# Kernel optimization log

Hardware: AMD Instinct MI355X
Metric: run time of the kernel (lower is better)

## Reference

```python
import jax, jax.numpy as jnp
import numpy as np

BN_EPS = 1e-5

def _tok2img(f):
    # f: [197, 768] tokens (CLS first). Drop CLS, transpose, reshape -> [1, 768, 14, 14].
    # fv4[0, c, i, j] = f[1 + i*14 + j, c], identical to the original triple loop.
    return f[1:].T.reshape(1, 768, 14, 14)

def _resize(x, s):
    # PyTorch F.interpolate(mode='bilinear', align_corners=False) == jax.image.resize 'bilinear'
    n, c, h, w = x.shape
    return jax.image.resize(x, (n, c, h * s, w * s), method='bilinear')

def _conv_relu_bn(x, conv_w, conv_b, g, b, m, v):
    y = jax.lax.conv_general_dilated(x, conv_w, window_strides=(1, 1), padding='SAME',
                                     dimension_numbers=('NCHW', 'OIHW', 'NCHW'))
    y = y + conv_b[None, :, None, None]
    y = jax.nn.relu(y)
    # BatchNorm2d(1) in eval mode with running stats
    scale = g * jax.lax.rsqrt(v + BN_EPS)
    return y * scale[None, :, None, None] + (b - m * scale)[None, :, None, None]

def setup_inputs() -> dict:
    key = jax.random.key(0)
    ks = jax.random.split(key, 4)
    return {
        'x': jax.random.normal(ks[0], (14, 14), dtype=jnp.float32),
        'fv': jax.random.normal(ks[1], (4, 197, 768), dtype=jnp.float32),
        'conv_w': jax.random.normal(ks[2], (1, 769, 3, 3), dtype=jnp.float32) * 0.02,
        'conv_b': jnp.zeros((1,), jnp.float32),
        'bn_gamma': jnp.ones((1,), jnp.float32),
        'bn_beta': jnp.zeros((1,), jnp.float32),
        'bn_mean': jnp.zeros((1,), jnp.float32),
        'bn_var': jnp.ones((1,), jnp.float32),
        'W_w': jax.random.normal(ks[3], (224, 224), dtype=jnp.float32) * 0.05,
        'W_b': jnp.zeros((224,), jnp.float32),
    }

def reference(x, fv, conv_w, conv_b, bn_gamma, bn_beta, bn_mean, bn_var, W_w, W_b):
    h = x[None, None]  # [1,1,14,14]
    # skip features, pre-resized to match current resolution at each stage
    feats = (
        _tok2img(fv[3]),              # 14x14
        _resize(_tok2img(fv[2]), 2),  # 28x28
        _resize(_tok2img(fv[1]), 4),  # 56x56
        _resize(_tok2img(fv[0]), 8),  # 112x112
    )
    for f in feats:
        h = jnp.concatenate([h, f], axis=1)  # [1,769,H,W]
        h = _conv_relu_bn(h, conv_w, conv_b, bn_gamma, bn_beta, bn_mean, bn_var)
        h = _resize(h, 2)
    # Linear(224,224) over the last dim of [1,1,224,224]
    h = jnp.einsum('nchw,ow->ncho', h, W_w) + W_b
    return jax.nn.sigmoid(h)
```

## Files before the change

kernel.cpp:

```cpp
#include <hip/hip_runtime.h>
#include <math.h>


#define BN_EPS 1e-5f

__device__ __forceinline__ float clampf(float x, float lo, float hi) {
    return fminf(fmaxf(x, lo), hi);
}

__device__ __forceinline__ float sampleB(const float* __restrict__ Bt, float fy, float fx) {
    int y0 = (int)fy; float by = fy - (float)y0; int y1 = min(y0 + 1, 13);
    int x0 = (int)fx; float bx = fx - (float)x0; int x1 = min(x0 + 1, 13);
    return (1.f - by) * ((1.f - bx) * Bt[y0 * 14 + x0] + bx * Bt[y0 * 14 + x1])
         + by         * ((1.f - bx) * Bt[y1 * 14 + x0] + bx * Bt[y1 * 14 + x1]);
}

__device__ __forceinline__ float stage_pixel(int i, int j, int H,
                                             const float* __restrict__ hsrc, int srcH,
                                             const float* __restrict__ sB,
                                             const float* __restrict__ cw, float bias) {
    float featScale = 14.0f / (float)H;
    float srcMax = (float)(srcH - 1);
    float acc = bias;

#pragma unroll
    for (int a = 0; a < 3; ++a) {
        int p = i + a - 1;
        if (p < 0 || p >= H) continue;
        float fy = clampf(((float)p + 0.5f) * featScale - 0.5f, 0.f, 13.f);
        float hy = clampf(((float)p + 0.5f) * 0.5f - 0.5f, 0.f, srcMax);
        int hy0 = (int)hy; float fhy = hy - (float)hy0; int hy1 = min(hy0 + 1, srcH - 1);
#pragma unroll
        for (int bq = 0; bq < 3; ++bq) {
            int q = j + bq - 1;
            if (q < 0 || q >= H) continue;
            int t = a * 3 + bq;

            float fx = clampf(((float)q + 0.5f) * featScale - 0.5f, 0.f, 13.f);
            float bv = sampleB(sB + t * 196, fy, fx);

            float hx = clampf(((float)q + 0.5f) * 0.5f - 0.5f, 0.f, srcMax);
            int hx0 = (int)hx; float fhx = hx - (float)hx0; int hx1 = min(hx0 + 1, srcH - 1);
            float hval = (1.f - fhy) * ((1.f - fhx) * hsrc[hy0 * srcH + hx0] + fhx * hsrc[hy0 * srcH + hx1])
                       + fhy         * ((1.f - fhx) * hsrc[hy1 * srcH + hx0] + fhx * hsrc[hy1 * srcH + hx1]);
            acc += cw[t] * hval + bv;
        }
    }
    return acc;
}

__device__ __forceinline__ void srcRange(int dlo, int dhi, int srcH, int& slo, int& shi) {
    int H = 2 * srcH;
    int p0 = max(dlo - 1, 0), p1 = min(dhi + 1, H - 1);
    float h0 = fmaxf(((float)p0 + 0.5f) * 0.5f - 0.5f, 0.f);
    float h1 = fmaxf(((float)p1 + 0.5f) * 0.5f - 0.5f, 0.f);
    slo = (int)h0;
    shi = min((int)h1 + 1, srcH - 1);
}

__device__ __forceinline__ void bRange(int dlo, int dhi, int H, int& lo, int& hi) {
    float sc = 14.f / (float)H;
    int p0 = max(dlo - 1, 0), p1 = min(dhi + 1, H - 1);
    float f0 = clampf(((float)p0 + 0.5f) * sc - 0.5f, 0.f, 13.f);
    float f1 = clampf(((float)p1 + 0.5f) * sc - 0.5f, 0.f, 13.f);
    lo = (int)f0;
    hi = min((int)f1 + 1, 13);
}

__global__ __launch_bounds__(256)
void compute_B_kernel(const float* __restrict__ fv, const float* __restrict__ conv_w,
                      const float* __restrict__ W_w,
                      float* __restrict__ gB, float* __restrict__ gWTf) {
    int blk = blockIdx.x;
    int s = blk / 196;
    int uv = blk % 196;
    const float* fvrow = fv + ((size_t)(3 - s) * 197 + 1 + uv) * 768;
    int tid = threadIdx.x;

    if (tid < 32) {
        int idx = blk * 32 + tid;
        int o = idx % 224, xx = idx / 224;
        float acc = 0.f;
#pragma unroll
        for (int d = -1; d <= 2; ++d) {
            int w = 2 * xx + d;
            if (w < 0 || w > 223) continue;
            float hx = clampf(((float)w + 0.5f) * 0.5f - 0.5f, 0.f, 111.f);
            int xx0 = (int)hx; float fx = hx - (float)xx0; int xx1 = min(xx0 + 1, 111);
            float c = (xx0 == xx ? 1.f - fx : 0.f) + (xx1 == xx ? fx : 0.f);
            acc += c * W_w[o * 224 + w];
        }
        gWTf[xx * 224 + o] = acc;
    }

    float part[9];
#pragma unroll
    for (int t = 0; t < 9; ++t) part[t] = 0.f;
    for (int k = tid; k < 768; k += 256) {
        float fval = fvrow[k];
        const float* w = conv_w + (size_t)(1 + k) * 9;
#pragma unroll
        for (int t = 0; t < 9; ++t) part[t] += fval * w[t];
    }
#pragma unroll
    for (int t = 0; t < 9; ++t) {
#pragma unroll
        for (int off = 32; off > 0; off >>= 1)
            part[t] += __shfl_down(part[t], off, 64);
    }
    __shared__ float red[4][9];
    int wave = tid >> 6, lane = tid & 63;
    if (lane == 0) {
#pragma unroll
        for (int t = 0; t < 9; ++t) red[wave][t] = part[t];
    }
    __syncthreads();
    if (tid < 9)
        gB[s * 1764 + tid * 196 + uv] = red[0][tid] + red[1][tid] + red[2][tid] + red[3][tid];
}

__global__ __launch_bounds__(1024, 1)
void refine_kernel(const float* __restrict__ x,
                   const float* __restrict__ conv_w, const float* __restrict__ conv_b,
                   const float* __restrict__ bng, const float* __restrict__ bnb,
                   const float* __restrict__ bnm, const float* __restrict__ bnv,
                   const float* __restrict__ W_b,
                   const float* __restrict__ gB, const float* __restrict__ gWTf,
                   float* __restrict__ out) {
    __shared__ float sB[4 * 9 * 196];
    __shared__ float y1s[196];
    __shared__ float y2s[784];
    __shared__ float y3s[3136];
    __shared__ float y4loc[3 * 112];
    __shared__ float partial[12 * 224];

    int tid = threadIdx.x;
    int b = blockIdx.x;

    int y4lo = max(b - 1, 0), y4hi = min(b + 1, 111);
    int r3lo, r3hi; srcRange(y4lo, y4hi, 56, r3lo, r3hi);
    int r2lo, r2hi; srcRange(r3lo, r3hi, 28, r2lo, r2hi);
    int r1lo, r1hi; srcRange(r2lo, r2hi, 14, r1lo, r1hi);

    int bl0 = max(r1lo - 1, 0), bh0 = min(r1hi + 1, 13);
    int bl1, bh1; bRange(r2lo, r2hi, 28, bl1, bh1);
    int bl2, bh2; bRange(r3lo, r3hi, 56, bl2, bh2);
    int bl3, bh3; bRange(y4lo, y4hi, 112, bl3, bh3);

    {
        int bl[4] = {bl0, bl1, bl2, bl3}, bh[4] = {bh0, bh1, bh2, bh3};
#pragma unroll
        for (int s4 = 0; s4 < 4; ++s4) {
            int nrw = (bh[s4] - bl[s4] + 1) * 14;
            int n = 9 * nrw;
            int base = s4 * 1764 + bl[s4] * 14;
            for (int e = tid; e < n; e += 1024) {
                int t = e / nrw, rem = e % nrw;
                int off = base + t * 196 + rem;
                sB[off] = gB[off];
            }
        }
    }

    float cw[9];
#pragma unroll
    for (int t = 0; t < 9; ++t) cw[t] = conv_w[t];
    float bias = conv_b[0];
    float scale = bng[0] * rsqrtf(bnv[0] + BN_EPS);
    float shift = bnb[0] - bnm[0] * scale;
    __syncthreads();

    {
        int n = (r1hi - r1lo + 1) * 14;
        if (tid < n) {
            int i = r1lo + tid / 14, j = tid % 14;
            float acc = bias;
#pragma unroll
            for (int a = 0; a < 3; ++a) {
                int p = i + a - 1;
                if (p < 0 || p >= 14) continue;
#pragma unroll
                for (int bq = 0; bq < 3; ++bq) {
                    int q = j + bq - 1;
                    if (q < 0 || q >= 14) continue;
                    int t = a * 3 + bq;
                    acc += cw[t] * x[p * 14 + q] + sB[t * 196 + p * 14 + q];
                }
            }
            y1s[i * 14 + j] = fmaxf(acc, 0.f) * scale + shift;
        }
    }
    __syncthreads();

    {
        int n = (r2hi - r2lo + 1) * 28;
        if (tid < n) {
            int i = r2lo + tid / 28, j = tid % 28;
            float acc = stage_pixel(i, j, 28, y1s, 14, sB + 1764, cw, bias);
            y2s[i * 28 + j] = fmaxf(acc, 0.f) * scale + shift;
        }
    }
    __syncthreads();

    {
        int n = (r3hi - r3lo + 1) * 56;
        if (tid < n) {
            int i = r3lo + tid / 56, j = tid % 56;
            float acc = stage_pixel(i, j, 56, y2s, 28, sB + 2 * 1764, cw, bias);
            y3s[i * 56 + j] = fmaxf(acc, 0.f) * scale + shift;
        }
    }
    __syncthreads();

    {
        int n = (y4hi - y4lo + 1) * 112;
        if (tid < n) {
            int i = y4lo + tid / 112, j = tid % 112;
            float acc = stage_pixel(i, j, 112, y3s, 56, sB + 3 * 1764, cw, bias);
            y4loc[(i - (b - 1)) * 112 + j] = fmaxf(acc, 0.f) * scale + shift;
        }
    }
    __syncthreads();

    if (tid < 896) {
        int kq = tid / 224, o = tid % 224;
        int k0 = kq * 28;
        float a0 = 0.f, a1 = 0.f, a2 = 0.f;
        for (int k = k0; k < k0 + 28; ++k) {
            float wf = gWTf[k * 224 + o];
            a0 += y4loc[k] * wf;
            a1 += y4loc[112 + k] * wf;
            a2 += y4loc[224 + k] * wf;
        }
        partial[(0 * 4 + kq) * 224 + o] = a0;
        partial[(1 * 4 + kq) * 224 + o] = a1;
        partial[(2 * 4 + kq) * 224 + o] = a2;
    }
    __syncthreads();

    if (tid < 448) {
        int rr = tid / 224, o = tid % 224;
        int r = 2 * b + rr;
        float hy = clampf(((float)r + 0.5f) * 0.5f - 0.5f, 0.f, 111.f);
        int yy0 = (int)hy; float fy = hy - (float)yy0; int yy1 = min(yy0 + 1, 111);
        int s0 = yy0 - (b - 1), s1 = yy1 - (b - 1);
        float D0 = partial[(s0 * 4 + 0) * 224 + o] + partial[(s0 * 4 + 1) * 224 + o]
                 + partial[(s0 * 4 + 2) * 224 + o] + partial[(s0 * 4 + 3) * 224 + o];
        float D1 = partial[(s1 * 4 + 0) * 224 + o] + partial[(s1 * 4 + 1) * 224 + o]
                 + partial[(s1 * 4 + 2) * 224 + o] + partial[(s1 * 4 + 3) * 224 + o];
        float v = (1.f - fy) * D0 + fy * D1 + W_b[o];
        out[(size_t)r * 224 + o] = 1.f / (1.f + expf(-v));
    }
}

extern "C" void kernel_launch(void* const* d_in, const int* in_sizes, int n_in,
                              void* d_out, int out_size, void* d_ws, size_t ws_size,
                              hipStream_t stream) {
    (void)in_sizes; (void)n_in; (void)out_size; (void)ws_size;
    const float* x      = (const float*)d_in[0];
    const float* fv     = (const float*)d_in[1];
    const float* conv_w = (const float*)d_in[2];
    const float* conv_b = (const float*)d_in[3];
    const float* bng    = (const float*)d_in[4];
    const float* bnb    = (const float*)d_in[5];
    const float* bnm    = (const float*)d_in[6];
    const float* bnv    = (const float*)d_in[7];
    const float* W_w    = (const float*)d_in[8];
    const float* W_b    = (const float*)d_in[9];
    float* out = (float*)d_out;

    float* ws   = (float*)d_ws;
    float* gB   = ws;
    float* gWTf = ws + 7056;

    compute_B_kernel<<<784, 256, 0, stream>>>(fv, conv_w, W_w, gB, gWTf);
    refine_kernel<<<112, 1024, 0, stream>>>(x, conv_w, conv_b, bng, bnb, bnm, bnv,
                                            W_b, gB, gWTf, out);
}
```

Measured before the change: 86.86 us.

## Fuse feature-projection precompute into refine kernel via cooperative grid sync

The separate compute_B kernel is merged into the refine kernel. Each of the 112 blocks computes seven feature-token projections and its own row of the folded linear weights, writes them to workspace, then waits on a cooperative grid-wide barrier before the refinement stages run. This removes a second kernel launch and the gap between launches. In exchange it depends on cooperative launch, pays for a grid sync, and uses fewer, larger blocks for the projection work.

```diff
diff --git a/kernel.cpp b/kernel.cpp
--- a/kernel.cpp
+++ b/kernel.cpp
@@ -1,5 +1,8 @@
 #include <hip/hip_runtime.h>
+#include <hip/hip_cooperative_groups.h>
 #include <math.h>
+
+namespace cg = cooperative_groups;
 
 
 #define BN_EPS 1e-5f
@@ -67,75 +70,77 @@
     hi = min((int)f1 + 1, 13);
 }
 
-__global__ __launch_bounds__(256)
-void compute_B_kernel(const float* __restrict__ fv, const float* __restrict__ conv_w,
-                      const float* __restrict__ W_w,
-                      float* __restrict__ gB, float* __restrict__ gWTf) {
-    int blk = blockIdx.x;
-    int s = blk / 196;
-    int uv = blk % 196;
-    const float* fvrow = fv + ((size_t)(3 - s) * 197 + 1 + uv) * 768;
-    int tid = threadIdx.x;
-
-    if (tid < 32) {
-        int idx = blk * 32 + tid;
-        int o = idx % 224, xx = idx / 224;
-        float acc = 0.f;
-#pragma unroll
-        for (int d = -1; d <= 2; ++d) {
-            int w = 2 * xx + d;
-            if (w < 0 || w > 223) continue;
-            float hx = clampf(((float)w + 0.5f) * 0.5f - 0.5f, 0.f, 111.f);
-            int xx0 = (int)hx; float fx = hx - (float)xx0; int xx1 = min(xx0 + 1, 111);
-            float c = (xx0 == xx ? 1.f - fx : 0.f) + (xx1 == xx ? fx : 0.f);
-            acc += c * W_w[o * 224 + w];
-        }
-        gWTf[xx * 224 + o] = acc;
-    }
-
-    float part[9];
-#pragma unroll
-    for (int t = 0; t < 9; ++t) part[t] = 0.f;
-    for (int k = tid; k < 768; k += 256) {
-        float fval = fvrow[k];
-        const float* w = conv_w + (size_t)(1 + k) * 9;
-#pragma unroll
-        for (int t = 0; t < 9; ++t) part[t] += fval * w[t];
-    }
-#pragma unroll
-    for (int t = 0; t < 9; ++t) {
-#pragma unroll
-        for (int off = 32; off > 0; off >>= 1)
-            part[t] += __shfl_down(part[t], off, 64);
-    }
-    __shared__ float red[4][9];
-    int wave = tid >> 6, lane = tid & 63;
-    if (lane == 0) {
-#pragma unroll
-        for (int t = 0; t < 9; ++t) red[wave][t] = part[t];
-    }
-    __syncthreads();
-    if (tid < 9)
-        gB[s * 1764 + tid * 196 + uv] = red[0][tid] + red[1][tid] + red[2][tid] + red[3][tid];
-}
-
 __global__ __launch_bounds__(1024, 1)
-void refine_kernel(const float* __restrict__ x,
-                   const float* __restrict__ conv_w, const float* __restrict__ conv_b,
-                   const float* __restrict__ bng, const float* __restrict__ bnb,
-                   const float* __restrict__ bnm, const float* __restrict__ bnv,
-                   const float* __restrict__ W_b,
-                   const float* __restrict__ gB, const float* __restrict__ gWTf,
-                   float* __restrict__ out) {
+void refine_fused(const float* __restrict__ x, const float* __restrict__ fv,
+                  const float* __restrict__ conv_w, const float* __restrict__ conv_b,
+                  const float* __restrict__ bng, const float* __restrict__ bnb,
+                  const float* __restrict__ bnm, const float* __restrict__ bnv,
+                  const float* __restrict__ W_w, const float* __restrict__ W_b,
+                  float* __restrict__ gB, float* __restrict__ gWTf,
+                  float* __restrict__ out) {
     __shared__ float sB[4 * 9 * 196];
     __shared__ float y1s[196];
     __shared__ float y2s[784];
     __shared__ float y3s[3136];
     __shared__ float y4loc[3 * 112];
     __shared__ float partial[12 * 224];
+    __shared__ float red[14][9];
 
     int tid = threadIdx.x;
     int b = blockIdx.x;
+
+    if (tid < 896) {
+        int e7 = tid >> 7, r = tid & 127;
+        int e = b * 7 + e7;
+        int s = e / 196, uv = e % 196;
+        const float* fvrow = fv + ((size_t)(3 - s) * 197 + 1 + uv) * 768;
+        float part[9];
+#pragma unroll
+        for (int t = 0; t < 9; ++t) part[t] = 0.f;
+#pragma unroll
+        for (int i = 0; i < 6; ++i) {
+            int c = r + 128 * i;
+            float fval = fvrow[c];
+            const float* w = conv_w + (size_t)(1 + c) * 9;
+#pragma unroll
+            for (int t = 0; t < 9; ++t) part[t] += fval * w[t];
+        }
+#pragma unroll
+        for (int t = 0; t < 9; ++t) {
+#pragma unroll
+            for (int off = 32; off > 0; off >>= 1)
+                part[t] += __shfl_down(part[t], off, 64);
+        }
+        if ((tid & 63) == 0) {
+            int wv = tid >> 6;
+#pragma unroll
+            for (int t = 0; t < 9; ++t) red[wv][t] = part[t];
+        }
+    }
+
+    if (tid < 224) {
+        int o = tid;
+        float acc = 0.f;
+#pragma unroll
+        for (int d = -1; d <= 2; ++d) {
+            int w = 2 * b + d;
+            if (w < 0 || w > 223) continue;
+            float hx = clampf(((float)w + 0.5f) * 0.5f - 0.5f, 0.f, 111.f);
+            int xx0 = (int)hx; float fx = hx - (float)xx0; int xx1 = min(xx0 + 1, 111);
+            float c = (xx0 == b ? 1.f - fx : 0.f) + (xx1 == b ? fx : 0.f);
+            acc += c * W_w[o * 224 + w];
+        }
+        gWTf[b * 224 + o] = acc;
+    }
+    __syncthreads();
+    if (tid < 63) {
+        int e7 = tid / 9, t = tid - e7 * 9;
+        int e = b * 7 + e7;
+        int s = e / 196, uv = e % 196;
+        gB[s * 1764 + t * 196 + uv] = red[2 * e7][t] + red[2 * e7 + 1][t];
+    }
+
+    cg::this_grid().sync();
 
     int y4lo = max(b - 1, 0), y4hi = min(b + 1, 111);
     int r3lo, r3hi; srcRange(y4lo, y4hi, 56, r3lo, r3hi);
@@ -273,7 +278,11 @@
     float* gB   = ws;
     float* gWTf = ws + 7056;
 
-    compute_B_kernel<<<784, 256, 0, stream>>>(fv, conv_w, W_w, gB, gWTf);
-    refine_kernel<<<112, 1024, 0, stream>>>(x, conv_w, conv_b, bng, bnb, bnm, bnv,
-                                            W_b, gB, gWTf, out);
-}
+    void* args[13] = {
+        (void*)&x, (void*)&fv, (void*)&conv_w, (void*)&conv_b,
+        (void*)&bng, (void*)&bnb, (void*)&bnm, (void*)&bnv,
+        (void*)&W_w, (void*)&W_b, (void*)&gB, (void*)&gWTf, (void*)&out
+    };
+    hipLaunchCooperativeKernel((void*)refine_fused, dim3(112), dim3(1024),
+                               args, 0, stream);
+}
```

Result: slower. 118.9 us (+36.9%).

## Fuse B and W-transform precompute into a single refine kernel

Applied to the files above, without the earlier changes.

Drops the separate precompute kernel. Each of the 112 blocks now computes only the feature-projection (B) entries its row window needs, one wave per token row with conv weights held in registers. It also builds the resized linear-weight matrix in shared memory instead of reading it from global workspace. This removes a kernel launch and the global round trip for intermediates. In exchange it adds redundant per-block recomputation, a large shared-memory footprint and heavy register pressure from the 108-element weight cache.

```diff
diff --git a/kernel.cpp b/kernel.cpp
--- a/kernel.cpp
+++ b/kernel.cpp
@@ -67,75 +67,24 @@
     hi = min((int)f1 + 1, 13);
 }
 
-__global__ __launch_bounds__(256)
-void compute_B_kernel(const float* __restrict__ fv, const float* __restrict__ conv_w,
-                      const float* __restrict__ W_w,
-                      float* __restrict__ gB, float* __restrict__ gWTf) {
-    int blk = blockIdx.x;
-    int s = blk / 196;
-    int uv = blk % 196;
-    const float* fvrow = fv + ((size_t)(3 - s) * 197 + 1 + uv) * 768;
-    int tid = threadIdx.x;
-
-    if (tid < 32) {
-        int idx = blk * 32 + tid;
-        int o = idx % 224, xx = idx / 224;
-        float acc = 0.f;
-#pragma unroll
-        for (int d = -1; d <= 2; ++d) {
-            int w = 2 * xx + d;
-            if (w < 0 || w > 223) continue;
-            float hx = clampf(((float)w + 0.5f) * 0.5f - 0.5f, 0.f, 111.f);
-            int xx0 = (int)hx; float fx = hx - (float)xx0; int xx1 = min(xx0 + 1, 111);
-            float c = (xx0 == xx ? 1.f - fx : 0.f) + (xx1 == xx ? fx : 0.f);
-            acc += c * W_w[o * 224 + w];
-        }
-        gWTf[xx * 224 + o] = acc;
-    }
-
-    float part[9];
-#pragma unroll
-    for (int t = 0; t < 9; ++t) part[t] = 0.f;
-    for (int k = tid; k < 768; k += 256) {
-        float fval = fvrow[k];
-        const float* w = conv_w + (size_t)(1 + k) * 9;
-#pragma unroll
-        for (int t = 0; t < 9; ++t) part[t] += fval * w[t];
-    }
-#pragma unroll
-    for (int t = 0; t < 9; ++t) {
-#pragma unroll
-        for (int off = 32; off > 0; off >>= 1)
-            part[t] += __shfl_down(part[t], off, 64);
-    }
-    __shared__ float red[4][9];
-    int wave = tid >> 6, lane = tid & 63;
-    if (lane == 0) {
-#pragma unroll
-        for (int t = 0; t < 9; ++t) red[wave][t] = part[t];
-    }
-    __syncthreads();
-    if (tid < 9)
-        gB[s * 1764 + tid * 196 + uv] = red[0][tid] + red[1][tid] + red[2][tid] + red[3][tid];
-}
-
 __global__ __launch_bounds__(1024, 1)
-void refine_kernel(const float* __restrict__ x,
-                   const float* __restrict__ conv_w, const float* __restrict__ conv_b,
-                   const float* __restrict__ bng, const float* __restrict__ bnb,
-                   const float* __restrict__ bnm, const float* __restrict__ bnv,
-                   const float* __restrict__ W_b,
-                   const float* __restrict__ gB, const float* __restrict__ gWTf,
-                   float* __restrict__ out) {
+void refine_one(const float* __restrict__ x, const float* __restrict__ fv,
+                const float* __restrict__ conv_w, const float* __restrict__ conv_b,
+                const float* __restrict__ bng, const float* __restrict__ bnb,
+                const float* __restrict__ bnm, const float* __restrict__ bnv,
+                const float* __restrict__ W_w, const float* __restrict__ W_b,
+                float* __restrict__ out) {
     __shared__ float sB[4 * 9 * 196];
     __shared__ float y1s[196];
     __shared__ float y2s[784];
     __shared__ float y3s[3136];
     __shared__ float y4loc[3 * 112];
     __shared__ float partial[12 * 224];
+    __shared__ float sWTf[112 * 224];
 
     int tid = threadIdx.x;
     int b = blockIdx.x;
+    int wave = tid >> 6, lane = tid & 63;
 
     int y4lo = max(b - 1, 0), y4hi = min(b + 1, 111);
     int r3lo, r3hi; srcRange(y4lo, y4hi, 56, r3lo, r3hi);
@@ -147,17 +96,49 @@
     int bl2, bh2; bRange(r3lo, r3hi, 56, bl2, bh2);
     int bl3, bh3; bRange(y4lo, y4hi, 112, bl3, bh3);
 
-    {
-        int bl[4] = {bl0, bl1, bl2, bl3}, bh[4] = {bh0, bh1, bh2, bh3};
-#pragma unroll
-        for (int s4 = 0; s4 < 4; ++s4) {
-            int nrw = (bh[s4] - bl[s4] + 1) * 14;
-            int n = 9 * nrw;
-            int base = s4 * 1764 + bl[s4] * 14;
-            for (int e = tid; e < n; e += 1024) {
-                int t = e / nrw, rem = e % nrw;
-                int off = base + t * 196 + rem;
-                sB[off] = gB[off];
+    int n0  = (bh0 - bl0 + 1) * 14;
+    int n1p = (bh1 - bl1 + 1) * 14;
+    int n2p = (bh2 - bl2 + 1) * 14;
+    int n3p = (bh3 - bl3 + 1) * 14;
+    int off1 = n0, off2 = n0 + n1p, off3 = n0 + n1p + n2p;
+    int Ne = off3 + n3p;
+
+    float cwreg[12][9];
+#pragma unroll
+    for (int i = 0; i < 12; ++i) {
+        const float* wp = conv_w + (size_t)(1 + lane + 64 * i) * 9;
+#pragma unroll
+        for (int t = 0; t < 9; ++t) cwreg[i][t] = wp[t];
+    }
+
+    {
+        int chunk = (Ne + 15) >> 4;
+        int e0 = wave * chunk, e1 = min(e0 + chunk, Ne);
+        for (int e = e0; e < e1; ++e) {
+            int s = (e >= off1) + (e >= off2) + (e >= off3);
+            int base = (s == 0) ? 0   : (s == 1) ? off1 : (s == 2) ? off2 : off3;
+            int bls  = (s == 0) ? bl0 : (s == 1) ? bl1  : (s == 2) ? bl2  : bl3;
+            int uv = bls * 14 + (e - base);
+            const float* fvrow = fv + ((size_t)(3 - s) * 197 + 1 + uv) * 768 + lane;
+            float acc[9];
+#pragma unroll
+            for (int t = 0; t < 9; ++t) acc[t] = 0.f;
+#pragma unroll
+            for (int i = 0; i < 12; ++i) {
+                float f = fvrow[64 * i];
+#pragma unroll
+                for (int t = 0; t < 9; ++t) acc[t] += cwreg[i][t] * f;
+            }
+#pragma unroll
+            for (int t = 0; t < 9; ++t) {
+#pragma unroll
+                for (int off = 32; off > 0; off >>= 1)
+                    acc[t] += __shfl_down(acc[t], off, 64);
+            }
+            if (lane == 0) {
+                int db = s * 1764 + uv;
+#pragma unroll
+                for (int t = 0; t < 9; ++t) sB[db + t * 196] = acc[t];
             }
         }
     }
@@ -170,10 +151,27 @@
     float shift = bnb[0] - bnm[0] * scale;
     __syncthreads();
 
-    {
+    if (tid < 896) {
+        int o = tid % 224;
+        int seg = tid / 224;
+        for (int xx = seg * 28; xx < seg * 28 + 28; ++xx) {
+            float acc = 0.f;
+#pragma unroll
+            for (int d = -1; d <= 2; ++d) {
+                int w = 2 * xx + d;
+                if (w < 0 || w > 223) continue;
+                float hx = clampf(((float)w + 0.5f) * 0.5f - 0.5f, 0.f, 111.f);
+                int xx0 = (int)hx; float fx = hx - (float)xx0; int xx1 = min(xx0 + 1, 111);
+                float c = (xx0 == xx ? 1.f - fx : 0.f) + (xx1 == xx ? fx : 0.f);
+                acc += c * W_w[o * 224 + w];
+            }
+            sWTf[xx * 224 + o] = acc;
+        }
+    } else {
+        int t2 = tid - 896;
         int n = (r1hi - r1lo + 1) * 14;
-        if (tid < n) {
-            int i = r1lo + tid / 14, j = tid % 14;
+        if (t2 < n) {
+            int i = r1lo + t2 / 14, j = t2 % 14;
             float acc = bias;
 #pragma unroll
             for (int a = 0; a < 3; ++a) {
@@ -227,7 +225,7 @@
         int k0 = kq * 28;
         float a0 = 0.f, a1 = 0.f, a2 = 0.f;
         for (int k = k0; k < k0 + 28; ++k) {
-            float wf = gWTf[k * 224 + o];
+            float wf = sWTf[k * 224 + o];
             a0 += y4loc[k] * wf;
             a1 += y4loc[112 + k] * wf;
             a2 += y4loc[224 + k] * wf;
@@ -256,7 +254,7 @@
 extern "C" void kernel_launch(void* const* d_in, const int* in_sizes, int n_in,
                               void* d_out, int out_size, void* d_ws, size_t ws_size,
                               hipStream_t stream) {
-    (void)in_sizes; (void)n_in; (void)out_size; (void)ws_size;
+    (void)in_sizes; (void)n_in; (void)out_size; (void)d_ws; (void)ws_size;
     const float* x      = (const float*)d_in[0];
     const float* fv     = (const float*)d_in[1];
     const float* conv_w = (const float*)d_in[2];
@@ -269,11 +267,6 @@
     const float* W_b    = (const float*)d_in[9];
     float* out = (float*)d_out;
 
-    float* ws   = (float*)d_ws;
-    float* gB   = ws;
-    float* gWTf = ws + 7056;
-
-    compute_B_kernel<<<784, 256, 0, stream>>>(fv, conv_w, W_w, gB, gWTf);
-    refine_kernel<<<112, 1024, 0, stream>>>(x, conv_w, conv_b, bng, bnb, bnm, bnv,
-                                            W_b, gB, gWTf, out);
-}
+    refine_one<<<112, 1024, 0, stream>>>(x, fv, conv_w, conv_b, bng, bnb,
+                                         bnm, bnv, W_w, W_b, out);
+}
```

Result: slower. 228.2 us (+162.8%).
